# Optimization experiments

Measured on AMD Instinct MI355X. Metric: run time of the kernel, lower is better.

## Reference

```python
import jax, jax.numpy as jnp
import numpy as np

B, T, D_IN = 32, 32, 128
N_SLOTS, M_LEN = 512, 64
NUM_SHIFT, NUM_READ, NUM_WRITE = 3, 4, 1
CTRL_DIM = 256
READ_HEAD_LEN = 3 + M_LEN + NUM_SHIFT            # k, beta, g, s, gamma
WRITE_HEAD_LEN = READ_HEAD_LEN + 2 * M_LEN       # + erase, add vectors
INSTR_DIM = NUM_READ * READ_HEAD_LEN + NUM_WRITE * WRITE_HEAD_LEN


def setup_inputs() -> dict:
    key = jax.random.key(0)
    ks = jax.random.split(key, 4)
    def glorot(k, shape):
        lim = np.sqrt(6.0 / (shape[0] + shape[1])).astype(np.float32)
        return jax.random.uniform(k, shape, jnp.float32, -lim, lim)
    return {
        "x": jax.random.normal(ks[0], (B, T, D_IN), jnp.float32),
        "Wc": glorot(ks[1], (D_IN + NUM_READ * M_LEN, CTRL_DIM)),
        "bc": jnp.zeros((CTRL_DIM,), jnp.float32),
        "heads_kernel": glorot(ks[2], (CTRL_DIM, INSTR_DIM)),
        "heads_bias": jnp.zeros((INSTR_DIM,), jnp.float32),
    }


def _parse_heads(h):
    # h: (B, H, 3 + M + S) -> k, beta, g, s, gamma per _get_weight_vector
    k = h[..., :M_LEN]
    b = jnp.exp(h[..., M_LEN])
    g = jax.nn.sigmoid(h[..., M_LEN + 1])
    s = jax.nn.softmax(h[..., M_LEN + 2:M_LEN + 2 + NUM_SHIFT], axis=-1)
    t = jax.nn.softplus(h[..., M_LEN + 2 + NUM_SHIFT]) + 1.0
    return k, b, g, s, t


def _address(Mem, w_prev, k, b, g, s, t):
    # Mem:(B,N,M) k:(B,H,M) w_prev:(B,H,N) b,g,t:(B,H) s:(B,H,S)
    eps = 1e-8
    Mn = jnp.linalg.norm(Mem, axis=-1)                       # (B,N)
    kn = jnp.linalg.norm(k, axis=-1)                         # (B,H)
    sim = jnp.einsum('bhm,bnm->bhn', k, Mem) / (kn[..., None] * Mn[:, None, :] + eps)
    wc = jax.nn.softmax(b[..., None] * sim, axis=-1)         # content
    wg = g[..., None] * wc + (1.0 - g[..., None]) * w_prev   # gate
    half = NUM_SHIFT // 2                                    # circular shift conv
    wsh = sum(s[..., i:i + 1] * jnp.roll(wg, i - half, axis=-1) for i in range(NUM_SHIFT))
    wt = wsh ** t[..., None]                                 # sharpen
    return wt / (jnp.sum(wt, axis=-1, keepdims=True) + eps)


def _ntm_forward(x, Wc, bc, heads_kernel, heads_bias):
    def step(carry, x_t):
        r, rw, ww, Mem = carry
        # dense controller on [x_t, old read vectors]
        ctrl_in = jnp.concatenate([x_t, r.reshape(B, -1)], axis=-1)
        h = jnp.tanh(ctrl_in @ Wc + bc)                      # controller_out == instr
        instr = h @ heads_kernel + heads_bias                # (B, INSTR_DIM)
        rh = instr[:, :NUM_READ * READ_HEAD_LEN].reshape(B, NUM_READ, READ_HEAD_LEN)
        wh = instr[:, NUM_READ * READ_HEAD_LEN:].reshape(B, NUM_WRITE, WRITE_HEAD_LEN)
        rw_n = _address(Mem, rw, *_parse_heads(rh))
        ww_n = _address(Mem, ww, *_parse_heads(wh[..., :READ_HEAD_LEN]))
        e = wh[..., READ_HEAD_LEN:READ_HEAD_LEN + M_LEN]     # raw erase (no sigmoid, as in source)
        a = wh[..., READ_HEAD_LEN + M_LEN:]                  # raw add
        # erase all heads, then add all heads (source loops erase first)
        Mem = Mem * jnp.prod(1.0 - ww_n[..., :, None] * e[..., None, :], axis=1)
        Mem = Mem + jnp.einsum('bwn,bwm->bnm', ww_n, a)
        r_n = jnp.einsum('bnm,brn->brm', Mem, rw_n)          # read
        return (r_n, rw_n, ww_n, Mem), h

    init = (jnp.zeros((B, NUM_READ, M_LEN), jnp.float32),
            jnp.zeros((B, NUM_READ, N_SLOTS), jnp.float32),
            jnp.zeros((B, NUM_WRITE, N_SLOTS), jnp.float32),
            jnp.zeros((B, N_SLOTS, M_LEN), jnp.float32))
    _, outs = jax.lax.scan(step, init, jnp.swapaxes(x, 0, 1))  # time-major
    return outs[-1]  # return_sequences=False -> last controller output (B, CTRL_DIM)


def reference(x, Wc, bc, heads_kernel, heads_bias):
    return _ntm_forward(x, Wc, bc, heads_kernel, heads_bias)
```

## Files before the change

### kernel.cpp

```cpp
#include <hip/hip_runtime.h>
#include <math.h>

#define BB 32
#define TT 32
#define D_INX 128
#define NSLOT 512
#define MLEN 64
#define NREAD 4
#define NHEAD 5
#define CDIM 256
#define IDIM 478
#define RHL 70
#define NT 512

#define HKB_OFF 196608

struct SMem {
    float mem[NSLOT * MLEN];
    float w4[NSLOT * 4];
    float ww[NSLOT];
    float mn[NSLOT];
    float ctrl[512];
    float h[CDIM];
    float instr[480];
    float k[NHEAD * MLEN];
    float e[MLEN];
    float a[MLEN];
    float u[NHEAD * NSLOT];
};

__device__ __forceinline__ unsigned short f2bf(float f) {
    unsigned u = __float_as_uint(f);
    return (unsigned short)((u + 0x7fffu + ((u >> 16) & 1u)) >> 16);
}

__device__ __forceinline__ float rlane(float v, int l) {
    return __int_as_float(__builtin_amdgcn_readlane(__float_as_int(v), l));
}

__global__ void pack_kernel(const float* __restrict__ Wc, const float* __restrict__ Hk,
                            unsigned short* __restrict__ wctb, unsigned short* __restrict__ hkb)
{
    int idx = blockIdx.x * 256 + threadIdx.x;
    if (idx < 384 * 256) {
        int i = idx >> 8, col = idx & 255;
        wctb[((i >> 3) * 256 + col) * 8 + (i & 7)] = f2bf(Wc[idx]);
    }
    if (idx < 256 * 478) {
        int i = idx / 478, col = idx - i * 478;
        hkb[((i >> 3) * 478 + col) * 8 + (i & 7)] = f2bf(Hk[idx]);
    }
}

#define BFS_DOT(wv, a0, a1, a2, a3, a4, a5, a6, a7, acc) do {                   \
    unsigned _u0 = __float_as_uint((wv).x), _u1 = __float_as_uint((wv).y);      \
    unsigned _u2 = __float_as_uint((wv).z), _u3 = __float_as_uint((wv).w);      \
    acc += __uint_as_float(_u0 << 16) * (a0) + __uint_as_float(_u0 & 0xffff0000u) * (a1); \
    acc += __uint_as_float(_u1 << 16) * (a2) + __uint_as_float(_u1 & 0xffff0000u) * (a3); \
    acc += __uint_as_float(_u2 << 16) * (a4) + __uint_as_float(_u2 & 0xffff0000u) * (a5); \
    acc += __uint_as_float(_u3 << 16) * (a6) + __uint_as_float(_u3 & 0xffff0000u) * (a7); \
} while (0)

#define P1_CHUNK(cg_) do {                                                      \
    float4 wv = wq[(cg_) * 256];                                                \
    const int k0 = (cg_) * 8;                                                   \
    float a0 = rlane(creg[(k0 + 0) >> 6], (k0 + 0) & 63);                       \
    float a1 = rlane(creg[(k0 + 1) >> 6], (k0 + 1) & 63);                       \
    float a2 = rlane(creg[(k0 + 2) >> 6], (k0 + 2) & 63);                       \
    float a3 = rlane(creg[(k0 + 3) >> 6], (k0 + 3) & 63);                       \
    float a4 = rlane(creg[(k0 + 4) >> 6], (k0 + 4) & 63);                       \
    float a5 = rlane(creg[(k0 + 5) >> 6], (k0 + 5) & 63);                       \
    float a6 = rlane(creg[(k0 + 6) >> 6], (k0 + 6) & 63);                       \
    float a7 = rlane(creg[(k0 + 7) >> 6], (k0 + 7) & 63);                       \
    BFS_DOT(wv, a0, a1, a2, a3, a4, a5, a6, a7, accs[(cg_) & 3]);               \
} while (0)

__global__ __launch_bounds__(NT, 2)
void ntm_kernel(const float* __restrict__ x,
                const float* __restrict__ bc,
                const float* __restrict__ hb,
                const unsigned short* __restrict__ wctb,
                const unsigned short* __restrict__ hkb,
                float* __restrict__ out)
{
    extern __shared__ float smem_f[];
    SMem* sc = (SMem*)smem_f;

    const int b    = blockIdx.x;
    const int tid  = threadIdx.x;
    const int lane = tid & 63;
    const int wave = tid >> 6;

    const int col   = tid & 255;
    const int halfw = tid >> 8;

    const float bcv = bc[col];
    const float hbv = (tid < IDIM) ? hb[tid] : 0.f;

    {
        float4 z4 = make_float4(0.f, 0.f, 0.f, 0.f);
        float4* m4 = (float4*)sc->mem;
        for (int i = tid; i < NSLOT * MLEN / 4; i += NT) m4[i] = z4;
        for (int i = tid; i < NSLOT * 4; i += NT) sc->w4[i] = 0.f;
        if (tid < NSLOT) sc->ww[tid] = 0.f;
        sc->ctrl[tid] = (tid < D_INX) ? x[(size_t)b * TT * D_INX + tid] : 0.f;
    }
    __syncthreads();

    for (int t = 0; t < TT; ++t) {
        {
            const bool xload = (tid < D_INX) && (t + 1 < TT);
            float xval = 0.f;
            if (xload) xval = x[((size_t)b * TT + t + 1) * D_INX + tid];

            const int xoff = (t & 1) ? 128 : 0;
            float creg[6];
            creg[0] = sc->ctrl[xoff + lane];
            creg[1] = sc->ctrl[xoff + 64 + lane];
            creg[2] = sc->ctrl[256 + lane];
            creg[3] = sc->ctrl[320 + lane];
            creg[4] = sc->ctrl[384 + lane];
            creg[5] = sc->ctrl[448 + lane];

            const float4* wq = (const float4*)wctb + col;
            float accs[4] = {0.f, 0.f, 0.f, 0.f};
            if (halfw == 0) {
#pragma unroll
                for (int cc = 0; cc < 24; ++cc) P1_CHUNK(cc);
            } else {
#pragma unroll
                for (int cc = 0; cc < 24; ++cc) P1_CHUNK(24 + cc);
            }
            float s = (accs[0] + accs[1]) + (accs[2] + accs[3]);
            if (halfw == 1) sc->u[col] = s;
            __syncthreads();
            if (halfw == 0) {
                float z = bcv + s + sc->u[col];
                z = fminf(fmaxf(z, -15.f), 15.f);
                float ex = __expf(2.f * z);
                float hv = (ex - 1.f) / (ex + 1.f);
                sc->h[col] = hv;
                if (t == TT - 1) out[(size_t)b * CDIM + col] = hv;
            }
            if (xload) sc->ctrl[((t + 1) & 1) * 128 + tid] = xval;
        }
        if (t == TT - 1) break;
        __syncthreads();

        {
            float hreg[4];
#pragma unroll
            for (int j = 0; j < 4; ++j) hreg[j] = sc->h[64 * j + lane];
            if (tid < IDIM) {
                const float4* wq2 = (const float4*)hkb + tid;
                float accs[4] = {0.f, 0.f, 0.f, 0.f};
#pragma unroll
                for (int c = 0; c < 32; ++c) {
                    float4 wv = wq2[c * 478];
                    const int k0 = c * 8;
                    float a0 = rlane(hreg[(k0 + 0) >> 6], (k0 + 0) & 63);
                    float a1 = rlane(hreg[(k0 + 1) >> 6], (k0 + 1) & 63);
                    float a2 = rlane(hreg[(k0 + 2) >> 6], (k0 + 2) & 63);
                    float a3 = rlane(hreg[(k0 + 3) >> 6], (k0 + 3) & 63);
                    float a4 = rlane(hreg[(k0 + 4) >> 6], (k0 + 4) & 63);
                    float a5 = rlane(hreg[(k0 + 5) >> 6], (k0 + 5) & 63);
                    float a6 = rlane(hreg[(k0 + 6) >> 6], (k0 + 6) & 63);
                    float a7 = rlane(hreg[(k0 + 7) >> 6], (k0 + 7) & 63);
                    BFS_DOT(wv, a0, a1, a2, a3, a4, a5, a6, a7, accs[c & 3]);
                }
                float acc = hbv + (accs[0] + accs[1]) + (accs[2] + accs[3]);
                sc->instr[tid] = acc;
                if (tid < 350) {
                    int hh = (tid * 937) >> 16;
                    int m = tid - hh * RHL;
                    if (m < MLEN) sc->k[hh * MLEN + m] = acc;
                } else if (tid < 414) {
                    sc->e[tid - 350] = acc;
                } else {
                    sc->a[tid - 414] = acc;
                }
            } else {
                for (int i = tid - IDIM; i < 256; i += NT - IDIM) sc->ctrl[256 + i] = 0.f;
            }
        }
        __syncthreads();

        {
            const int n = tid, nx = n & 15;
            const float4* m4 = (const float4*)sc->mem + n * 16;
            float kreg[5];
#pragma unroll
            for (int h2 = 0; h2 < 5; ++h2) kreg[h2] = sc->k[h2 * MLEN + lane];
            float d0 = 0.f, d1 = 0.f, d2 = 0.f, d3 = 0.f, d4 = 0.f, nsq = 0.f;
#pragma unroll
            for (int j = 0; j < 16; ++j) {
                float4 mv = m4[j ^ nx];
                nsq += mv.x * mv.x + mv.y * mv.y + mv.z * mv.z + mv.w * mv.w;
                d0 += mv.x * rlane(kreg[0], 4*j) + mv.y * rlane(kreg[0], 4*j+1)
                    + mv.z * rlane(kreg[0], 4*j+2) + mv.w * rlane(kreg[0], 4*j+3);
                d1 += mv.x * rlane(kreg[1], 4*j) + mv.y * rlane(kreg[1], 4*j+1)
                    + mv.z * rlane(kreg[1], 4*j+2) + mv.w * rlane(kreg[1], 4*j+3);
                d2 += mv.x * rlane(kreg[2], 4*j) + mv.y * rlane(kreg[2], 4*j+1)
                    + mv.z * rlane(kreg[2], 4*j+2) + mv.w * rlane(kreg[2], 4*j+3);
                d3 += mv.x * rlane(kreg[3], 4*j) + mv.y * rlane(kreg[3], 4*j+1)
                    + mv.z * rlane(kreg[3], 4*j+2) + mv.w * rlane(kreg[3], 4*j+3);
                d4 += mv.x * rlane(kreg[4], 4*j) + mv.y * rlane(kreg[4], 4*j+1)
                    + mv.z * rlane(kreg[4], 4*j+2) + mv.w * rlane(kreg[4], 4*j+3);
            }
            sc->u[n] = d0; sc->u[NSLOT + n] = d1; sc->u[2 * NSLOT + n] = d2;
            sc->u[3 * NSLOT + n] = d3; sc->u[4 * NSLOT + n] = d4;
            sc->mn[n] = sqrtf(nsq);
        }
        __syncthreads();

        if (wave < NHEAD) {
            const int h = wave;
            const float* ins = sc->instr + h * RHL;
            float kv = ins[lane];
            float sq = kv * kv;
#pragma unroll
            for (int off = 32; off; off >>= 1) sq += __shfl_xor(sq, off);
            float kn = sqrtf(sq);
            float beta = __expf(ins[64]);
            float g = 1.f / (1.f + __expf(-ins[65]));
            float v0 = ins[66], v1 = ins[67], v2 = ins[68];
            float mx3 = fmaxf(v0, fmaxf(v1, v2));
            float e0 = __expf(v0 - mx3), e1 = __expf(v1 - mx3), e2 = __expf(v2 - mx3);
            float inv3 = 1.f / (e0 + e1 + e2);
            float s0 = e0 * inv3, s1 = e1 * inv3, s2 = e2 * inv3;
            float tv = ins[69];
            float tp = fmaxf(tv, 0.f) + log1pf(__expf(-fabsf(tv))) + 1.f;

            float uu[8];
#pragma unroll
            for (int j = 0; j < 8; ++j) {
                int slot = j * 64 + lane;
                float d = sc->u[h * NSLOT + slot];
                uu[j] = beta * d / (kn * sc->mn[slot] + 1e-8f);
            }
            float m = uu[0];
#pragma unroll
            for (int j = 1; j < 8; ++j) m = fmaxf(m, uu[j]);
#pragma unroll
            for (int off = 32; off; off >>= 1) m = fmaxf(m, __shfl_xor(m, off));
            float ev[8]; float Z = 0.f;
#pragma unroll
            for (int j = 0; j < 8; ++j) { ev[j] = __expf(uu[j] - m); Z += ev[j]; }
#pragma unroll
            for (int off = 32; off; off >>= 1) Z += __shfl_xor(Z, off);
            float invZ = 1.f / Z;
            float wg[8];
#pragma unroll
            for (int j = 0; j < 8; ++j) {
                int slot = j * 64 + lane;
                float oldw = (h < 4) ? sc->w4[slot * 4 + h] : sc->ww[slot];
                wg[j] = g * ev[j] * invZ + (1.f - g) * oldw;
            }
            int lm = (lane + 63) & 63, lp = (lane + 1) & 63;
            float rm[8], rp[8];
#pragma unroll
            for (int j = 0; j < 8; ++j) {
                float sm = (lane == 63) ? wg[(j + 7) & 7] : wg[j];
                float sp = (lane == 0)  ? wg[(j + 1) & 7] : wg[j];
                rm[j] = __shfl(sm, lm);
                rp[j] = __shfl(sp, lp);
            }
            float wt[8]; float S = 0.f;
#pragma unroll
            for (int j = 0; j < 8; ++j) {
                float wsh = s0 * rp[j] + s1 * wg[j] + s2 * rm[j];
                wt[j] = __builtin_amdgcn_exp2f(tp * __builtin_amdgcn_logf(wsh));
                S += wt[j];
            }
#pragma unroll
            for (int off = 32; off; off >>= 1) S += __shfl_xor(S, off);
            float invS = 1.f / (S + 1e-8f);
#pragma unroll
            for (int j = 0; j < 8; ++j) {
                int slot = j * 64 + lane;
                float wnew = wt[j] * invS;
                if (h < 4) sc->w4[slot * 4 + h] = wnew;
                else       sc->ww[slot] = wnew;
            }
        }
        __syncthreads();

        {
            const int rg = lane >> 4, j = lane & 15, base = wave * 64;
            const float4 ev = ((const float4*)sc->e)[j];
            const float4 av = ((const float4*)sc->a)[j];
            float4* m4 = (float4*)sc->mem;
            float4 ac[4];
#pragma unroll
            for (int hh = 0; hh < 4; ++hh) ac[hh] = make_float4(0.f, 0.f, 0.f, 0.f);
#pragma unroll
            for (int i = 0; i < 16; ++i) {
                const int n = base + 4 * i + rg;
                const int idx = n * 16 + (j ^ (n & 15));
                float4 mv = m4[idx];
                const float wv = sc->ww[n];
                mv.x = mv.x * (1.f - wv * ev.x) + wv * av.x;
                mv.y = mv.y * (1.f - wv * ev.y) + wv * av.y;
                mv.z = mv.z * (1.f - wv * ev.z) + wv * av.z;
                mv.w = mv.w * (1.f - wv * ev.w) + wv * av.w;
                m4[idx] = mv;
                const float4 w4v = ((const float4*)sc->w4)[n];
                ac[0].x += w4v.x * mv.x; ac[0].y += w4v.x * mv.y; ac[0].z += w4v.x * mv.z; ac[0].w += w4v.x * mv.w;
                ac[1].x += w4v.y * mv.x; ac[1].y += w4v.y * mv.y; ac[1].z += w4v.y * mv.z; ac[1].w += w4v.y * mv.w;
                ac[2].x += w4v.z * mv.x; ac[2].y += w4v.z * mv.y; ac[2].z += w4v.z * mv.z; ac[2].w += w4v.z * mv.w;
                ac[3].x += w4v.w * mv.x; ac[3].y += w4v.w * mv.y; ac[3].z += w4v.w * mv.z; ac[3].w += w4v.w * mv.w;
            }
            float* af = (float*)ac;
#pragma unroll
            for (int q = 0; q < 16; ++q) {
                af[q] += __shfl_xor(af[q], 16);
                af[q] += __shfl_xor(af[q], 32);
            }
            if (rg == 0) {
#pragma unroll
                for (int hh = 0; hh < 4; ++hh) {
                    atomicAdd(&sc->ctrl[256 + hh * 64 + 4 * j + 0], ac[hh].x);
                    atomicAdd(&sc->ctrl[256 + hh * 64 + 4 * j + 1], ac[hh].y);
                    atomicAdd(&sc->ctrl[256 + hh * 64 + 4 * j + 2], ac[hh].z);
                    atomicAdd(&sc->ctrl[256 + hh * 64 + 4 * j + 3], ac[hh].w);
                }
            }
        }
        __syncthreads();
    }
}

extern "C" void kernel_launch(void* const* d_in, const int* in_sizes, int n_in,
                              void* d_out, int out_size, void* d_ws, size_t ws_size,
                              hipStream_t stream) {
    const float* x  = (const float*)d_in[0];
    const float* Wc = (const float*)d_in[1];
    const float* bc = (const float*)d_in[2];
    const float* Hk = (const float*)d_in[3];
    const float* hb = (const float*)d_in[4];
    float* out = (float*)d_out;

    unsigned short* wctb = (unsigned short*)d_ws;
    unsigned short* hkb  = (unsigned short*)((char*)d_ws + HKB_OFF);

    static_assert(sizeof(SMem) <= 163840, "LDS overflow");
    (void)hipFuncSetAttribute((const void*)ntm_kernel,
                              hipFuncAttributeMaxDynamicSharedMemorySize,
                              (int)sizeof(SMem));

    hipLaunchKernelGGL(pack_kernel, dim3(478), dim3(256), 0, stream, Wc, Hk, wctb, hkb);
    hipLaunchKernelGGL(ntm_kernel, dim3(BB), dim3(NT), sizeof(SMem), stream,
                       x, bc, hb, wctb, hkb, out);
}
```

Baseline: 880.5 us.

## Double block size to 1024 threads and split phases across more waves

Raises the workgroup from 512 to 1024 threads. The controller matvec is now split four ways over the input dimension, with partial sums reduced through shared memory. The memory-norm computation now runs alongside the heads matvec, and the five-key similarity is split across two thread groups. The memory update/read loop now handles half as many rows per wave. The goal is more parallelism per sequential timestep, at the cost of register pressure under the tighter launch bounds, an extra barrier, and an unshown read-reduction tail that must handle 16 waves.

```diff
diff --git a/kernel.cpp b/kernel.cpp
--- a/kernel.cpp
+++ b/kernel.cpp
@@ -11,7 +11,7 @@
 #define CDIM 256
 #define IDIM 478
 #define RHL 70
-#define NT 512
+#define NT 1024
 
 #define HKB_OFF 196608
 
@@ -75,7 +75,7 @@
     BFS_DOT(wv, a0, a1, a2, a3, a4, a5, a6, a7, accs[(cg_) & 3]);               \
 } while (0)
 
-__global__ __launch_bounds__(NT, 2)
+__global__ __launch_bounds__(NT, 4)
 void ntm_kernel(const float* __restrict__ x,
                 const float* __restrict__ bc,
                 const float* __restrict__ hb,
@@ -91,8 +91,8 @@
     const int lane = tid & 63;
     const int wave = tid >> 6;
 
-    const int col   = tid & 255;
-    const int halfw = tid >> 8;
+    const int col     = tid & 255;
+    const int quarter = tid >> 8;
 
     const float bcv = bc[col];
     const float hbv = (tid < IDIM) ? hb[tid] : 0.f;
@@ -103,7 +103,7 @@
         for (int i = tid; i < NSLOT * MLEN / 4; i += NT) m4[i] = z4;
         for (int i = tid; i < NSLOT * 4; i += NT) sc->w4[i] = 0.f;
         if (tid < NSLOT) sc->ww[tid] = 0.f;
-        sc->ctrl[tid] = (tid < D_INX) ? x[(size_t)b * TT * D_INX + tid] : 0.f;
+        if (tid < 512) sc->ctrl[tid] = (tid < D_INX) ? x[(size_t)b * TT * D_INX + tid] : 0.f;
     }
     __syncthreads();
 
@@ -124,18 +124,24 @@
 
             const float4* wq = (const float4*)wctb + col;
             float accs[4] = {0.f, 0.f, 0.f, 0.f};
-            if (halfw == 0) {
-#pragma unroll
-                for (int cc = 0; cc < 24; ++cc) P1_CHUNK(cc);
+            if (quarter == 0) {
+#pragma unroll
+                for (int cc = 0; cc < 12; ++cc) P1_CHUNK(cc);
+            } else if (quarter == 1) {
+#pragma unroll
+                for (int cc = 0; cc < 12; ++cc) P1_CHUNK(12 + cc);
+            } else if (quarter == 2) {
+#pragma unroll
+                for (int cc = 0; cc < 12; ++cc) P1_CHUNK(24 + cc);
             } else {
 #pragma unroll
-                for (int cc = 0; cc < 24; ++cc) P1_CHUNK(24 + cc);
+                for (int cc = 0; cc < 12; ++cc) P1_CHUNK(36 + cc);
             }
             float s = (accs[0] + accs[1]) + (accs[2] + accs[3]);
-            if (halfw == 1) sc->u[col] = s;
+            if (quarter != 0) sc->u[1024 + quarter * 256 + col] = s;
             __syncthreads();
-            if (halfw == 0) {
-                float z = bcv + s + sc->u[col];
+            if (quarter == 0) {
+                float z = bcv + s + sc->u[1280 + col] + sc->u[1536 + col] + sc->u[1792 + col];
                 z = fminf(fmaxf(z, -15.f), 15.f);
                 float ex = __expf(2.f * z);
                 float hv = (ex - 1.f) / (ex + 1.f);
@@ -147,7 +153,7 @@
         if (t == TT - 1) break;
         __syncthreads();
 
-        {
+        if (tid < 512) {
             float hreg[4];
 #pragma unroll
             for (int j = 0; j < 4; ++j) hreg[j] = sc->h[64 * j + lane];
@@ -180,36 +186,55 @@
                     sc->a[tid - 414] = acc;
                 }
             } else {
-                for (int i = tid - IDIM; i < 256; i += NT - IDIM) sc->ctrl[256 + i] = 0.f;
-            }
-        }
-        __syncthreads();
-
-        {
-            const int n = tid, nx = n & 15;
+                for (int i = tid - IDIM; i < 256; i += 512 - IDIM) sc->ctrl[256 + i] = 0.f;
+            }
+        } else {
+            const int n = tid - 512, nx = n & 15;
             const float4* m4 = (const float4*)sc->mem + n * 16;
-            float kreg[5];
-#pragma unroll
-            for (int h2 = 0; h2 < 5; ++h2) kreg[h2] = sc->k[h2 * MLEN + lane];
-            float d0 = 0.f, d1 = 0.f, d2 = 0.f, d3 = 0.f, d4 = 0.f, nsq = 0.f;
+            float nsq = 0.f;
 #pragma unroll
             for (int j = 0; j < 16; ++j) {
                 float4 mv = m4[j ^ nx];
                 nsq += mv.x * mv.x + mv.y * mv.y + mv.z * mv.z + mv.w * mv.w;
-                d0 += mv.x * rlane(kreg[0], 4*j) + mv.y * rlane(kreg[0], 4*j+1)
-                    + mv.z * rlane(kreg[0], 4*j+2) + mv.w * rlane(kreg[0], 4*j+3);
-                d1 += mv.x * rlane(kreg[1], 4*j) + mv.y * rlane(kreg[1], 4*j+1)
-                    + mv.z * rlane(kreg[1], 4*j+2) + mv.w * rlane(kreg[1], 4*j+3);
-                d2 += mv.x * rlane(kreg[2], 4*j) + mv.y * rlane(kreg[2], 4*j+1)
-                    + mv.z * rlane(kreg[2], 4*j+2) + mv.w * rlane(kreg[2], 4*j+3);
-                d3 += mv.x * rlane(kreg[3], 4*j) + mv.y * rlane(kreg[3], 4*j+1)
-                    + mv.z * rlane(kreg[3], 4*j+2) + mv.w * rlane(kreg[3], 4*j+3);
-                d4 += mv.x * rlane(kreg[4], 4*j) + mv.y * rlane(kreg[4], 4*j+1)
-                    + mv.z * rlane(kreg[4], 4*j+2) + mv.w * rlane(kreg[4], 4*j+3);
-            }
-            sc->u[n] = d0; sc->u[NSLOT + n] = d1; sc->u[2 * NSLOT + n] = d2;
-            sc->u[3 * NSLOT + n] = d3; sc->u[4 * NSLOT + n] = d4;
+            }
             sc->mn[n] = sqrtf(nsq);
+        }
+        __syncthreads();
+
+        {
+            const int n = tid & 511, nx = n & 15;
+            const int grp = tid >> 9;
+            const float4* m4 = (const float4*)sc->mem + n * 16;
+            if (grp == 0) {
+                float k0r = sc->k[lane];
+                float k1r = sc->k[64 + lane];
+                float k2r = sc->k[128 + lane];
+                float d0 = 0.f, d1 = 0.f, d2 = 0.f;
+#pragma unroll
+                for (int j = 0; j < 16; ++j) {
+                    float4 mv = m4[j ^ nx];
+                    d0 += mv.x * rlane(k0r, 4*j) + mv.y * rlane(k0r, 4*j+1)
+                        + mv.z * rlane(k0r, 4*j+2) + mv.w * rlane(k0r, 4*j+3);
+                    d1 += mv.x * rlane(k1r, 4*j) + mv.y * rlane(k1r, 4*j+1)
+                        + mv.z * rlane(k1r, 4*j+2) + mv.w * rlane(k1r, 4*j+3);
+                    d2 += mv.x * rlane(k2r, 4*j) + mv.y * rlane(k2r, 4*j+1)
+                        + mv.z * rlane(k2r, 4*j+2) + mv.w * rlane(k2r, 4*j+3);
+                }
+                sc->u[n] = d0; sc->u[NSLOT + n] = d1; sc->u[2 * NSLOT + n] = d2;
+            } else {
+                float k3r = sc->k[192 + lane];
+                float k4r = sc->k[256 + lane];
+                float d3 = 0.f, d4 = 0.f;
+#pragma unroll
+                for (int j = 0; j < 16; ++j) {
+                    float4 mv = m4[j ^ nx];
+                    d3 += mv.x * rlane(k3r, 4*j) + mv.y * rlane(k3r, 4*j+1)
+                        + mv.z * rlane(k3r, 4*j+2) + mv.w * rlane(k3r, 4*j+3);
+                    d4 += mv.x * rlane(k4r, 4*j) + mv.y * rlane(k4r, 4*j+1)
+                        + mv.z * rlane(k4r, 4*j+2) + mv.w * rlane(k4r, 4*j+3);
+                }
+                sc->u[3 * NSLOT + n] = d3; sc->u[4 * NSLOT + n] = d4;
+            }
         }
         __syncthreads();
 
@@ -286,7 +311,7 @@
         __syncthreads();
 
         {
-            const int rg = lane >> 4, j = lane & 15, base = wave * 64;
+            const int rg = lane >> 4, j = lane & 15, base = wave * 32;
             const float4 ev = ((const float4*)sc->e)[j];
             const float4 av = ((const float4*)sc->a)[j];
             float4* m4 = (float4*)sc->mem;
@@ -294,7 +319,7 @@
 #pragma unroll
             for (int hh = 0; hh < 4; ++hh) ac[hh] = make_float4(0.f, 0.f, 0.f, 0.f);
 #pragma unroll
-            for (int i = 0; i < 16; ++i) {
+            for (int i = 0; i < 8; ++i) {
                 const int n = base + 4 * i + rg;
                 const int idx = n * 16 + (j ^ (n & 15));
                 float4 mv = m4[idx];
```

After: 1.108 ms. 25.9% more time.

## Precompute input projection in separate kernel and switch weights from bf16 to fp32

Applied to the files above, without the earlier changes.

The x_t·Wc[:128] part of the controller matmul plus its bias is moved out of the sequential time loop into a parallel xpart_kernel that writes a per-(b,t) projection buffer. The recurrent loop now only multiplies the 256 read-vector entries. The packed weights also change from bf16 to fp32, which removes the rounding error but doubles the global/L2 weight traffic each step. An extra kernel launch and a workspace buffer are added.

```diff
diff --git a/kernel.cpp b/kernel.cpp
--- a/kernel.cpp
+++ b/kernel.cpp
@@ -13,14 +13,16 @@
 #define RHL 70
 #define NT 512
 
-#define HKB_OFF 196608
+#define XP_SZ   1048576
+#define WCT_OFF XP_SZ
+#define HKB_OFF (XP_SZ + 262144)
 
 struct SMem {
     float mem[NSLOT * MLEN];
     float w4[NSLOT * 4];
     float ww[NSLOT];
     float mn[NSLOT];
-    float ctrl[512];
+    float ctrl[256];
     float h[CDIM];
     float instr[480];
     float k[NHEAD * MLEN];
@@ -29,40 +31,41 @@
     float u[NHEAD * NSLOT];
 };
 
-__device__ __forceinline__ unsigned short f2bf(float f) {
-    unsigned u = __float_as_uint(f);
-    return (unsigned short)((u + 0x7fffu + ((u >> 16) & 1u)) >> 16);
-}
-
 __device__ __forceinline__ float rlane(float v, int l) {
     return __int_as_float(__builtin_amdgcn_readlane(__float_as_int(v), l));
 }
 
 __global__ void pack_kernel(const float* __restrict__ Wc, const float* __restrict__ Hk,
-                            unsigned short* __restrict__ wctb, unsigned short* __restrict__ hkb)
+                            float* __restrict__ wct, float* __restrict__ hkb)
 {
     int idx = blockIdx.x * 256 + threadIdx.x;
-    if (idx < 384 * 256) {
+    if (idx < 256 * 256) {
         int i = idx >> 8, col = idx & 255;
-        wctb[((i >> 3) * 256 + col) * 8 + (i & 7)] = f2bf(Wc[idx]);
+        wct[((i >> 3) * 256 + col) * 8 + (i & 7)] = Wc[(128 + i) * 256 + col];
     }
     if (idx < 256 * 478) {
         int i = idx / 478, col = idx - i * 478;
-        hkb[((i >> 3) * 478 + col) * 8 + (i & 7)] = f2bf(Hk[idx]);
+        hkb[((i >> 3) * 478 + col) * 8 + (i & 7)] = Hk[i * 478 + col];
     }
 }
 
-#define BFS_DOT(wv, a0, a1, a2, a3, a4, a5, a6, a7, acc) do {                   \
-    unsigned _u0 = __float_as_uint((wv).x), _u1 = __float_as_uint((wv).y);      \
-    unsigned _u2 = __float_as_uint((wv).z), _u3 = __float_as_uint((wv).w);      \
-    acc += __uint_as_float(_u0 << 16) * (a0) + __uint_as_float(_u0 & 0xffff0000u) * (a1); \
-    acc += __uint_as_float(_u1 << 16) * (a2) + __uint_as_float(_u1 & 0xffff0000u) * (a3); \
-    acc += __uint_as_float(_u2 << 16) * (a4) + __uint_as_float(_u2 & 0xffff0000u) * (a5); \
-    acc += __uint_as_float(_u3 << 16) * (a6) + __uint_as_float(_u3 & 0xffff0000u) * (a7); \
-} while (0)
+__global__ __launch_bounds__(256)
+void xpart_kernel(const float* __restrict__ x, const float* __restrict__ Wc,
+                  const float* __restrict__ bc, float* __restrict__ xp)
+{
+    __shared__ float xs[D_INX];
+    const int bt = blockIdx.x, col = threadIdx.x;
+    if (col < D_INX) xs[col] = x[(size_t)bt * D_INX + col];
+    __syncthreads();
+    float acc = bc[col];
+#pragma unroll 8
+    for (int k = 0; k < D_INX; ++k) acc += xs[k] * Wc[k * 256 + col];
+    xp[(size_t)bt * CDIM + col] = acc;
+}
 
 #define P1_CHUNK(cg_) do {                                                      \
-    float4 wv = wq[(cg_) * 256];                                                \
+    const float4 w0 = wqa[(cg_) * 512];                                         \
+    const float4 w1 = wqa[(cg_) * 512 + 1];                                     \
     const int k0 = (cg_) * 8;                                                   \
     float a0 = rlane(creg[(k0 + 0) >> 6], (k0 + 0) & 63);                       \
     float a1 = rlane(creg[(k0 + 1) >> 6], (k0 + 1) & 63);                       \
@@ -72,15 +75,15 @@
     float a5 = rlane(creg[(k0 + 5) >> 6], (k0 + 5) & 63);                       \
     float a6 = rlane(creg[(k0 + 6) >> 6], (k0 + 6) & 63);                       \
     float a7 = rlane(creg[(k0 + 7) >> 6], (k0 + 7) & 63);                       \
-    BFS_DOT(wv, a0, a1, a2, a3, a4, a5, a6, a7, accs[(cg_) & 3]);               \
+    accs[(cg_) & 3] += w0.x * a0 + w0.y * a1 + w0.z * a2 + w0.w * a3            \
+                     + w1.x * a4 + w1.y * a5 + w1.z * a6 + w1.w * a7;           \
 } while (0)
 
 __global__ __launch_bounds__(NT, 2)
-void ntm_kernel(const float* __restrict__ x,
-                const float* __restrict__ bc,
+void ntm_kernel(const float* __restrict__ xp,
                 const float* __restrict__ hb,
-                const unsigned short* __restrict__ wctb,
-                const unsigned short* __restrict__ hkb,
+                const float* __restrict__ wct,
+                const float* __restrict__ hkb,
                 float* __restrict__ out)
 {
     extern __shared__ float smem_f[];
@@ -94,7 +97,6 @@
     const int col   = tid & 255;
     const int halfw = tid >> 8;
 
-    const float bcv = bc[col];
     const float hbv = (tid < IDIM) ? hb[tid] : 0.f;
 
     {
@@ -103,46 +105,40 @@
         for (int i = tid; i < NSLOT * MLEN / 4; i += NT) m4[i] = z4;
         for (int i = tid; i < NSLOT * 4; i += NT) sc->w4[i] = 0.f;
         if (tid < NSLOT) sc->ww[tid] = 0.f;
-        sc->ctrl[tid] = (tid < D_INX) ? x[(size_t)b * TT * D_INX + tid] : 0.f;
+        if (tid < 256) sc->ctrl[tid] = 0.f;
     }
     __syncthreads();
 
     for (int t = 0; t < TT; ++t) {
         {
-            const bool xload = (tid < D_INX) && (t + 1 < TT);
-            float xval = 0.f;
-            if (xload) xval = x[((size_t)b * TT + t + 1) * D_INX + tid];
-
-            const int xoff = (t & 1) ? 128 : 0;
-            float creg[6];
-            creg[0] = sc->ctrl[xoff + lane];
-            creg[1] = sc->ctrl[xoff + 64 + lane];
-            creg[2] = sc->ctrl[256 + lane];
-            creg[3] = sc->ctrl[320 + lane];
-            creg[4] = sc->ctrl[384 + lane];
-            creg[5] = sc->ctrl[448 + lane];
-
-            const float4* wq = (const float4*)wctb + col;
+            const float xpv = xp[(size_t)(b * TT + t) * CDIM + col];
+
+            float creg[4];
+            creg[0] = sc->ctrl[lane];
+            creg[1] = sc->ctrl[64 + lane];
+            creg[2] = sc->ctrl[128 + lane];
+            creg[3] = sc->ctrl[192 + lane];
+
+            const float4* wqa = (const float4*)wct + col * 2;
             float accs[4] = {0.f, 0.f, 0.f, 0.f};
             if (halfw == 0) {
 #pragma unroll
-                for (int cc = 0; cc < 24; ++cc) P1_CHUNK(cc);
+                for (int cc = 0; cc < 16; ++cc) P1_CHUNK(cc);
             } else {
 #pragma unroll
-                for (int cc = 0; cc < 24; ++cc) P1_CHUNK(24 + cc);
+                for (int cc = 0; cc < 16; ++cc) P1_CHUNK(16 + cc);
             }
             float s = (accs[0] + accs[1]) + (accs[2] + accs[3]);
             if (halfw == 1) sc->u[col] = s;
             __syncthreads();
             if (halfw == 0) {
-                float z = bcv + s + sc->u[col];
+                float z = xpv + s + sc->u[col];
                 z = fminf(fmaxf(z, -15.f), 15.f);
                 float ex = __expf(2.f * z);
                 float hv = (ex - 1.f) / (ex + 1.f);
                 sc->h[col] = hv;
                 if (t == TT - 1) out[(size_t)b * CDIM + col] = hv;
             }
-            if (xload) sc->ctrl[((t + 1) & 1) * 128 + tid] = xval;
         }
         if (t == TT - 1) break;
         __syncthreads();
@@ -152,11 +148,12 @@
 #pragma unroll
             for (int j = 0; j < 4; ++j) hreg[j] = sc->h[64 * j + lane];
             if (tid < IDIM) {
-                const float4* wq2 = (const float4*)hkb + tid;
+                const float4* wq2a = (const float4*)hkb + tid * 2;
                 float accs[4] = {0.f, 0.f, 0.f, 0.f};
 #pragma unroll
                 for (int c = 0; c < 32; ++c) {
-                    float4 wv = wq2[c * 478];
+                    const float4 w0 = wq2a[c * 956];
+                    const float4 w1 = wq2a[c * 956 + 1];
                     const int k0 = c * 8;
                     float a0 = rlane(hreg[(k0 + 0) >> 6], (k0 + 0) & 63);
                     float a1 = rlane(hreg[(k0 + 1) >> 6], (k0 + 1) & 63);
@@ -166,7 +163,8 @@
                     float a5 = rlane(hreg[(k0 + 5) >> 6], (k0 + 5) & 63);
                     float a6 = rlane(hreg[(k0 + 6) >> 6], (k0 + 6) & 63);
                     float a7 = rlane(hreg[(k0 + 7) >> 6], (k0 + 7) & 63);
-                    BFS_DOT(wv, a0, a1, a2, a3, a4, a5, a6, a7, accs[c & 3]);
+                    accs[c & 3] += w0.x * a0 + w0.y * a1 + w0.z * a2 + w0.w * a3
+                                 + w1.x * a4 + w1.y * a5 + w1.z * a6 + w1.w * a7;
                 }
                 float acc = hbv + (accs[0] + accs[1]) + (accs[2] + accs[3]);
                 sc->instr[tid] = acc;
@@ -180,7 +178,7 @@
                     sc->a[tid - 414] = acc;
                 }
             } else {
-                for (int i = tid - IDIM; i < 256; i += NT - IDIM) sc->ctrl[256 + i] = 0.f;
+                for (int i = tid - IDIM; i < 256; i += NT - IDIM) sc->ctrl[i] = 0.f;
             }
         }
         __syncthreads();
@@ -319,10 +317,10 @@
             if (rg == 0) {
 #pragma unroll
                 for (int hh = 0; hh < 4; ++hh) {
-                    atomicAdd(&sc->ctrl[256 + hh * 64 + 4 * j + 0], ac[hh].x);
-                    atomicAdd(&sc->ctrl[256 + hh * 64 + 4 * j + 1], ac[hh].y);
-                    atomicAdd(&sc->ctrl[256 + hh * 64 + 4 * j + 2], ac[hh].z);
-                    atomicAdd(&sc->ctrl[256 + hh * 64 + 4 * j + 3], ac[hh].w);
+                    atomicAdd(&sc->ctrl[hh * 64 + 4 * j + 0], ac[hh].x);
+                    atomicAdd(&sc->ctrl[hh * 64 + 4 * j + 1], ac[hh].y);
+                    atomicAdd(&sc->ctrl[hh * 64 + 4 * j + 2], ac[hh].z);
+                    atomicAdd(&sc->ctrl[hh * 64 + 4 * j + 3], ac[hh].w);
                 }
             }
         }
@@ -340,15 +338,17 @@
     const float* hb = (const float*)d_in[4];
     float* out = (float*)d_out;
 
-    unsigned short* wctb = (unsigned short*)d_ws;
-    unsigned short* hkb  = (unsigned short*)((char*)d_ws + HKB_OFF);
+    float* xp  = (float*)d_ws;
+    float* wct = (float*)((char*)d_ws + WCT_OFF);
+    float* hkb = (float*)((char*)d_ws + HKB_OFF);
 
     static_assert(sizeof(SMem) <= 163840, "LDS overflow");
     (void)hipFuncSetAttribute((const void*)ntm_kernel,
                               hipFuncAttributeMaxDynamicSharedMemorySize,
                               (int)sizeof(SMem));
 
-    hipLaunchKernelGGL(pack_kernel, dim3(478), dim3(256), 0, stream, Wc, Hk, wctb, hkb);
+    hipLaunchKernelGGL(pack_kernel, dim3(478), dim3(256), 0, stream, Wc, Hk, wct, hkb);
+    hipLaunchKernelGGL(xpart_kernel, dim3(BB * TT), dim3(256), 0, stream, x, Wc, bc, xp);
     hipLaunchKernelGGL(ntm_kernel, dim3(BB), dim3(NT), sizeof(SMem), stream,
-                       x, bc, hb, wctb, hkb, out);
-}
+                       xp, hb, wct, hkb, out);
+}
```

Measured after the change: 772.4 us. 1.14x faster.
